# Optimization experiments

Measured on AMD Instinct MI355X. Metric: run time of the kernel, lower is better.

Reference implementation:

```python
import jax, jax.numpy as jnp
import numpy as np

B = 8192          # batch (tokens)
D_LAT = 1024      # latent_dim
D_EMB = 1024      # embed_dim
D = D_LAT + D_EMB # input_dim = 2048
E = 8             # num_experts
K = 2             # top-k


def setup_inputs() -> dict:
    key = jax.random.key(0)
    ks = jax.random.split(key, 6)
    s = 1.0 / np.sqrt(D)  # PyTorch nn.Linear init bound
    return {
        "x": jax.random.normal(ks[0], (B, D_LAT), dtype=jnp.float32),
        "y": jax.random.normal(ks[1], (B, D_EMB), dtype=jnp.float32),
        # expert Linear weights [E, out=D, in=D] and biases [E, D]
        "W_experts": jax.random.uniform(ks[2], (E, D, D), jnp.float32, -s, s),
        "b_experts": jax.random.uniform(ks[3], (E, D), jnp.float32, -s, s),
        # gate Linear weight [E, D] and bias [E]
        "W_gate": jax.random.uniform(ks[4], (E, D), jnp.float32, -s, s),
        "b_gate": jax.random.uniform(ks[5], (E,), jnp.float32, -s, s),
    }


def reference(x, y, W_experts, b_experts, W_gate, b_gate):
    # inp: [B, D]
    inp = jnp.concatenate([x, y], axis=1)
    # gating (eval mode: no noise): [B, E]
    gate_logits = inp @ W_gate.T + b_gate
    # top-k values/indices (sorted descending, matching torch.topk): [B, K]
    topk_val, topk_idx = jax.lax.top_k(gate_logits, K)
    topk_gates = jax.nn.softmax(topk_val, axis=1)  # [B, K]
    # dense all-expert outputs, matching original per-expert loop: [B, E, D]
    all_out = jnp.einsum('bd,eod->beo', inp, W_experts) + b_experts[None, :, :]
    # gather top-k expert outputs: [B, K, D]
    topk_out = jnp.take_along_axis(all_out, topk_idx[:, :, None], axis=1)
    # gate-weighted combine: [B, D]
    fused = jnp.sum(topk_out * topk_gates[:, :, None], axis=1)
    return fused
```

## Files before the change

kernel.cpp:

```cpp
#include <hip/hip_runtime.h>
#include <stdint.h>

typedef __attribute__((ext_vector_type(4))) float f32x4;
typedef __attribute__((ext_vector_type(8))) short short8v;
typedef __attribute__((ext_vector_type(8))) unsigned short ushort8v;
typedef __attribute__((ext_vector_type(4))) unsigned short ushort4v;

#define NB 8192
#define ND 2048
#define NE 8
#define NT 32

__device__ __forceinline__ unsigned short f2bf(float f) {
    union { float f; uint32_t u; } c; c.f = f;
    uint32_t u = c.u;
    u = u + 0x7FFFu + ((u >> 16) & 1u);
    return (unsigned short)(u >> 16);
}

__global__ __launch_bounds__(256) void cvt_w_kernel(const float* __restrict__ W,
                                                    unsigned short* __restrict__ Wb) {
    size_t i = ((size_t)blockIdx.x * 256 + threadIdx.x) * 8;
    float4 a = *(const float4*)(W + i);
    float4 b = *(const float4*)(W + i + 4);
    ushort8v o;
    o[0] = f2bf(a.x); o[1] = f2bf(a.y); o[2] = f2bf(a.z); o[3] = f2bf(a.w);
    o[4] = f2bf(b.x); o[5] = f2bf(b.y); o[6] = f2bf(b.z); o[7] = f2bf(b.w);
    *(ushort8v*)(Wb + i) = o;
}

__global__ __launch_bounds__(256) void gatecvt_kernel(const float* __restrict__ x,
                                                      const float* __restrict__ y,
                                                      const float* __restrict__ Wg,
                                                      const float* __restrict__ bg,
                                                      unsigned short* __restrict__ inpb,
                                                      int* __restrict__ tkidx,
                                                      float* __restrict__ tkg) {
    const int wave = threadIdx.x >> 6, lane = threadIdx.x & 63;
    const int b = blockIdx.x * 4 + wave;
    const float* xb = x + (size_t)b * 1024;
    const float* yb = y + (size_t)b * 1024;
    unsigned short* ob = inpb + (size_t)b * ND;
    double acc[NE] = {0, 0, 0, 0, 0, 0, 0, 0};
#pragma unroll
    for (int it = 0; it < 8; it++) {
        const int d = it * 256 + lane * 4;
        float4 v = (it < 4) ? *(const float4*)(xb + d) : *(const float4*)(yb + (d - 1024));
        ushort4v o;
        o[0] = f2bf(v.x); o[1] = f2bf(v.y); o[2] = f2bf(v.z); o[3] = f2bf(v.w);
        *(ushort4v*)(ob + d) = o;
#pragma unroll
        for (int e = 0; e < NE; e++) {
            float4 w = *(const float4*)(Wg + e * ND + d);
            acc[e] += (double)v.x * (double)w.x + (double)v.y * (double)w.y
                    + (double)v.z * (double)w.z + (double)v.w * (double)w.w;
        }
    }
#pragma unroll
    for (int e = 0; e < NE; e++) {
        double s = acc[e];
#pragma unroll
        for (int o = 32; o >= 1; o >>= 1) s += __shfl_xor(s, o, 64);
        acc[e] = s;
    }
    if (lane == 0) {
        double v0 = -1e300, v1 = -1e300; int i0 = 0, i1 = 1;
#pragma unroll
        for (int e = 0; e < NE; e++) {
            double val = acc[e] + (double)bg[e];
            if (val > v0)      { v1 = v0; i1 = i0; v0 = val; i0 = e; }
            else if (val > v1) { v1 = val; i1 = e; }
        }
        double e1 = exp(v1 - v0);
        double inv = 1.0 / (1.0 + e1);
        tkidx[b * 2]     = i0;
        tkidx[b * 2 + 1] = i1;
        tkg[b * 2]       = (float)inv;
        tkg[b * 2 + 1]   = (float)(e1 * inv);
    }
}

__global__ __launch_bounds__(256) void hist_kernel(const int* __restrict__ tkidx,
                                                   int* __restrict__ hist) {
    const int p = blockIdx.x * 256 + threadIdx.x;
    const int wave = threadIdx.x >> 6, lane = threadIdx.x & 63;
    const int e = tkidx[p];
    __shared__ int cnt[4][8];
#pragma unroll
    for (int e2 = 0; e2 < 8; e2++) {
        unsigned long long m = __ballot(e == e2);
        if (lane == e2) cnt[wave][e2] = __popcll(m);
    }
    __syncthreads();
    if (threadIdx.x < 8)
        hist[blockIdx.x * 8 + threadIdx.x] =
            cnt[0][threadIdx.x] + cnt[1][threadIdx.x] + cnt[2][threadIdx.x] + cnt[3][threadIdx.x];
}

__global__ void scan_kernel(const int* __restrict__ hist, int* __restrict__ chunkbase,
                            int* __restrict__ meta) {
    __shared__ int total[8], off[8];
    const int t = threadIdx.x;
    if (t < 8) {
        int run = 0;
        for (int c = 0; c < 64; c++) { chunkbase[c * 8 + t] = run; run += hist[c * 8 + t]; }
        total[t] = run; meta[t] = run;
    }
    __syncthreads();
    if (t == 0) { int o = 0; for (int e = 0; e < 8; e++) { off[e] = o; meta[8 + e] = o; o += total[e]; } }
    __syncthreads();
    for (int i = t; i < 512; i += 64) chunkbase[i] += off[i & 7];
}

__global__ __launch_bounds__(256) void fill_kernel(const int* __restrict__ tkidx,
                                                   const float* __restrict__ tkg,
                                                   const int* __restrict__ chunkbase,
                                                   int* __restrict__ tok,
                                                   float* __restrict__ gat) {
    const int p = blockIdx.x * 256 + threadIdx.x;
    const int wave = threadIdx.x >> 6, lane = threadIdx.x & 63;
    const int e = tkidx[p];
    const float g = tkg[p];
    __shared__ int cnt[4][8];
    unsigned long long mym = 0;
#pragma unroll
    for (int e2 = 0; e2 < 8; e2++) {
        unsigned long long m = __ballot(e == e2);
        if (e == e2) mym = m;
        if (lane == e2) cnt[wave][e2] = __popcll(m);
    }
    __syncthreads();
    int basep = chunkbase[blockIdx.x * 8 + e];
    for (int w = 0; w < wave; w++) basep += cnt[w][e];
    const int rank = __popcll(mym & ((1ull << lane) - 1ull));
    tok[basep + rank] = p;
    gat[basep + rank] = g;
}

__global__ __launch_bounds__(256) void combine_kernel(float* __restrict__ out,
                                                      const float* __restrict__ part1) {
    const size_t stride = (size_t)gridDim.x * 256 * 4;
    for (size_t i = ((size_t)blockIdx.x * 256 + threadIdx.x) * 4;
         i < (size_t)NB * ND; i += stride) {
        f32x4 a = *(const f32x4*)(out + i);
        f32x4 b = *(const f32x4*)(part1 + i);
        a = a + b;
        *(f32x4*)(out + i) = a;
    }
}

#define GLD16(gp, lp) __builtin_amdgcn_global_load_lds( \
    (const __attribute__((address_space(1))) uint32_t*)(gp), \
    (__attribute__((address_space(3))) uint32_t*)(lp), 16, 0, 0)

template <bool STORE>
__global__ __launch_bounds__(512, 2) void moe_gemm_kernel(
    const unsigned short* __restrict__ Ab,
    const unsigned short* __restrict__ Wb,
    const float* __restrict__ bias,
    const int* __restrict__ tok,
    const float* __restrict__ gat,
    const int* __restrict__ meta,
    float* __restrict__ out0,
    float* __restrict__ out1)
{
    const int e = blockIdx.z;
    const int cnt = meta[e];
    const int row0 = blockIdx.y * 256;
    if (row0 >= cnt) return;
    const int col0 = blockIdx.x * 256;
    const int base = meta[8 + e];

    __shared__ __align__(16) unsigned short S[2][4][128][64];

    const int tid  = threadIdx.x;
    const int wv   = tid >> 6;
    const int lane = tid & 63;
    const int wr = wv >> 2, wcn = wv & 3;
    const int fr = lane & 15, kh = lane >> 4;

    const int srow = tid >> 3;
    const int cg8  = ((tid & 7) ^ (srow & 7)) * 8;
    const unsigned short* wbase = Wb + (size_t)e * ND * ND;
    const unsigned short* aptr[2][2];
    const unsigned short* bptr[2][2];
#pragma unroll
    for (int h = 0; h < 2; h++)
#pragma unroll
        for (int i = 0; i < 2; i++) {
            int rt = h * 128 + i * 64 + srow;
            int gr = row0 + rt; if (gr > cnt - 1) gr = cnt - 1;
            aptr[h][i] = Ab + (size_t)(tok[base + gr] >> 1) * ND + cg8;
            bptr[h][i] = wbase + (size_t)(col0 + rt) * ND + cg8;
        }

#define STAGE_A(SB, SM, SK) do { \
    GLD16(aptr[SM][0] + (SK), (char*)&S[SB][SM][0][0] + tid * 16); \
    GLD16(aptr[SM][1] + (SK), (char*)&S[SB][SM][0][0] + tid * 16 + 8192); } while (0)
#define STAGE_B(SB, SN, SK) do { \
    GLD16(bptr[SN][0] + (SK), (char*)&S[SB][2 + SN][0][0] + tid * 16); \
    GLD16(bptr[SN][1] + (SK), (char*)&S[SB][2 + SN][0][0] + tid * 16 + 8192); } while (0)
#define STAGE_ALL(SB, SK) do { \
    STAGE_A(SB, 0, SK); STAGE_B(SB, 0, SK); STAGE_B(SB, 1, SK); STAGE_A(SB, 1, SK); } while (0)

    f32x4 acc[8][4];
#pragma unroll
    for (int m = 0; m < 8; m++)
#pragma unroll
        for (int n = 0; n < 4; n++) acc[m][n] = f32x4{0.f, 0.f, 0.f, 0.f};

    const int arow = wr * 64 + fr;
    int ca[2];
#pragma unroll
    for (int ks = 0; ks < 2; ks++) ca[ks] = ((ks * 4 + kh) ^ (fr & 7)) * 8;

#define LD_A(PB, PM, ML, KS) (*(const short8v*)&S[PB][PM][arow + (ML) * 16][ca[KS]])
#define LD_B(PB, N, KS)      (*(const short8v*)&S[PB][2 + ((N) >> 1)][wcn * 32 + ((N) & 1) * 16 + fr][ca[KS]])
#define MFMA16(MQ) do { \
    __builtin_amdgcn_s_setprio(1); \
    _Pragma("unroll") \
    for (int ml = 0; ml < 4; ml++) \
        _Pragma("unroll") \
        for (int n = 0; n < 4; n++) \
            acc[(MQ) * 4 + ml][n] = __builtin_amdgcn_mfma_f32_16x16x32_bf16( \
                ar[ml], br[n], acc[(MQ) * 4 + ml][n], 0, 0, 0); \
    __builtin_amdgcn_s_setprio(0); \
    __builtin_amdgcn_sched_barrier(0); \
} while (0)

#define BODY(PB) do { \
    short8v ar[4], br[4]; \
    _Pragma("unroll") \
    for (int i = 0; i < 4; i++) ar[i] = LD_A(PB, 0, i, 0); \
    _Pragma("unroll") \
    for (int i = 0; i < 4; i++) br[i] = LD_B(PB, i, 0); \
    MFMA16(0); \
    _Pragma("unroll") \
    for (int i = 0; i < 4; i++) ar[i] = LD_A(PB, 1, i, 0); \
    MFMA16(1); \
    _Pragma("unroll") \
    for (int i = 0; i < 4; i++) ar[i] = LD_A(PB, 0, i, 1); \
    _Pragma("unroll") \
    for (int i = 0; i < 4; i++) br[i] = LD_B(PB, i, 1); \
    MFMA16(0); \
    _Pragma("unroll") \
    for (int i = 0; i < 4; i++) ar[i] = LD_A(PB, 1, i, 1); \
    MFMA16(1); \
} while (0)

    STAGE_ALL(0, 0);
    __syncthreads();

    for (int t = 0; t < NT; t += 2) {
        if (t + 1 < NT) STAGE_ALL(1, (t + 1) * 64);
        BODY(0);
        __syncthreads();
        if (t + 2 < NT) STAGE_ALL(0, (t + 2) * 64);
        BODY(1);
        __syncthreads();
    }

    int   coln[4];
    float bv[4];
#pragma unroll
    for (int n = 0; n < 4; n++) {
        coln[n] = col0 + (n >> 1) * 128 + wcn * 32 + (n & 1) * 16 + fr;
        bv[n] = bias[e * ND + coln[n]];
    }
#pragma unroll
    for (int m = 0; m < 8; m++) {
        const int rbase = row0 + (m >> 2) * 128 + wr * 64 + (m & 3) * 16 + kh * 4;
#pragma unroll
        for (int j = 0; j < 4; j++) {
            const int R = rbase + j;
            if (R < cnt) {
                const int pr = tok[base + R];
                const float g = gat[base + R];
                float* orow = ((STORE && (pr & 1)) ? out1 : out0) + (size_t)(pr >> 1) * ND;
#pragma unroll
                for (int n = 0; n < 4; n++) {
                    const float v = g * (acc[m][n][j] + bv[n]);
                    if (STORE) orow[coln[n]] = v;
                    else       atomicAdd(&orow[coln[n]], v);
                }
            }
        }
    }
#undef BODY
#undef MFMA16
#undef LD_A
#undef LD_B
#undef STAGE_ALL
#undef STAGE_A
#undef STAGE_B
}

extern "C" void kernel_launch(void* const* d_in, const int* in_sizes, int n_in,
                              void* d_out, int out_size, void* d_ws, size_t ws_size,
                              hipStream_t stream) {
    const float* x  = (const float*)d_in[0];
    const float* y  = (const float*)d_in[1];
    const float* We = (const float*)d_in[2];
    const float* be = (const float*)d_in[3];
    const float* Wg = (const float*)d_in[4];
    const float* bg = (const float*)d_in[5];
    float* out = (float*)d_out;

    char* ws = (char*)d_ws;
    int*   meta  = (int*)ws;
    int*   hist  = (int*)(ws + 256);
    int*   cbase = (int*)(ws + 256 + 2048);
    int*   tkidx = (int*)(ws + 8192);
    float* tkg   = (float*)(ws + 8192 + 65536);
    int*   tok   = (int*)(ws + 8192 + 2 * 65536);
    float* gat   = (float*)(ws + 8192 + 3 * 65536);
    const size_t off_inpb = 8192 + 4 * 65536;
    const size_t off_wb   = off_inpb + (size_t)NB * ND * 2;
    const size_t off_p1   = off_wb + (size_t)NE * ND * ND * 2;
    const size_t needed   = off_p1 + (size_t)NB * ND * 4;
    unsigned short* inpb = (unsigned short*)(ws + off_inpb);
    unsigned short* wb   = (unsigned short*)(ws + off_wb);
    float*          part1 = (float*)(ws + off_p1);
    const bool store_mode = (ws_size >= needed);

    cvt_w_kernel<<<16384, 256, 0, stream>>>(We, wb);
    gatecvt_kernel<<<2048, 256, 0, stream>>>(x, y, Wg, bg, inpb, tkidx, tkg);
    hist_kernel<<<64, 256, 0, stream>>>(tkidx, hist);
    scan_kernel<<<1, 64, 0, stream>>>(hist, cbase, meta);
    fill_kernel<<<64, 256, 0, stream>>>(tkidx, tkg, cbase, tok, gat);
    if (store_mode) {
        moe_gemm_kernel<true><<<dim3(8, 32, 8), 512, 0, stream>>>(inpb, wb, be, tok, gat, meta, out, part1);
        combine_kernel<<<2048, 256, 0, stream>>>(out, part1);
    } else {
        (void)hipMemsetAsync(d_out, 0, (size_t)NB * ND * sizeof(float), stream);
        moe_gemm_kernel<false><<<dim3(8, 32, 8), 512, 0, stream>>>(inpb, wb, be, tok, gat, meta, out, out);
    }
}
```

Baseline: 291.7 us.

## Merge routing kernels into one block and preload B fragments in GEMM

Result: slower. 446.1 us (+53.0%).

```diff
diff --git a/kernel.cpp b/kernel.cpp
--- a/kernel.cpp
+++ b/kernel.cpp
@@ -80,61 +80,48 @@
     }
 }
 
-__global__ __launch_bounds__(256) void hist_kernel(const int* __restrict__ tkidx,
-                                                   int* __restrict__ hist) {
-    const int p = blockIdx.x * 256 + threadIdx.x;
-    const int wave = threadIdx.x >> 6, lane = threadIdx.x & 63;
-    const int e = tkidx[p];
-    __shared__ int cnt[4][8];
+__global__ __launch_bounds__(1024) void bucket_kernel(const int* __restrict__ tkidx,
+                                                      const float* __restrict__ tkg,
+                                                      int* __restrict__ meta,
+                                                      int* __restrict__ tok,
+                                                      float* __restrict__ gat) {
+    __shared__ int hist[1024][8];
+    __shared__ int ebase[8];
+    const int t = threadIdx.x;
+    int loc[16];
+#pragma unroll
+    for (int i = 0; i < 16; i++) loc[i] = tkidx[t * 16 + i];
 #pragma unroll
     for (int e2 = 0; e2 < 8; e2++) {
-        unsigned long long m = __ballot(e == e2);
-        if (lane == e2) cnt[wave][e2] = __popcll(m);
+        int c = 0;
+#pragma unroll
+        for (int i = 0; i < 16; i++) c += (loc[i] == e2) ? 1 : 0;
+        hist[t][e2] = c;
     }
     __syncthreads();
-    if (threadIdx.x < 8)
-        hist[blockIdx.x * 8 + threadIdx.x] =
-            cnt[0][threadIdx.x] + cnt[1][threadIdx.x] + cnt[2][threadIdx.x] + cnt[3][threadIdx.x];
-}
-
-__global__ void scan_kernel(const int* __restrict__ hist, int* __restrict__ chunkbase,
-                            int* __restrict__ meta) {
-    __shared__ int total[8], off[8];
-    const int t = threadIdx.x;
     if (t < 8) {
         int run = 0;
-        for (int c = 0; c < 64; c++) { chunkbase[c * 8 + t] = run; run += hist[c * 8 + t]; }
-        total[t] = run; meta[t] = run;
+        for (int j = 0; j < 1024; j++) { int v = hist[j][t]; hist[j][t] = run; run += v; }
+        meta[t] = run;
     }
     __syncthreads();
-    if (t == 0) { int o = 0; for (int e = 0; e < 8; e++) { off[e] = o; meta[8 + e] = o; o += total[e]; } }
+    if (t == 0) {
+        int o = 0;
+        for (int e = 0; e < 8; e++) { ebase[e] = o; meta[8 + e] = o; o += meta[e]; }
+    }
     __syncthreads();
-    for (int i = t; i < 512; i += 64) chunkbase[i] += off[i & 7];
-}
-
-__global__ __launch_bounds__(256) void fill_kernel(const int* __restrict__ tkidx,
-                                                   const float* __restrict__ tkg,
-                                                   const int* __restrict__ chunkbase,
-                                                   int* __restrict__ tok,
-                                                   float* __restrict__ gat) {
-    const int p = blockIdx.x * 256 + threadIdx.x;
-    const int wave = threadIdx.x >> 6, lane = threadIdx.x & 63;
-    const int e = tkidx[p];
-    const float g = tkg[p];
-    __shared__ int cnt[4][8];
-    unsigned long long mym = 0;
 #pragma unroll
     for (int e2 = 0; e2 < 8; e2++) {
-        unsigned long long m = __ballot(e == e2);
-        if (e == e2) mym = m;
-        if (lane == e2) cnt[wave][e2] = __popcll(m);
-    }
-    __syncthreads();
-    int basep = chunkbase[blockIdx.x * 8 + e];
-    for (int w = 0; w < wave; w++) basep += cnt[w][e];
-    const int rank = __popcll(mym & ((1ull << lane) - 1ull));
-    tok[basep + rank] = p;
-    gat[basep + rank] = g;
+        int pp = ebase[e2] + hist[t][e2];
+#pragma unroll
+        for (int i = 0; i < 16; i++) {
+            if (loc[i] == e2) {
+                tok[pp] = t * 16 + i;
+                gat[pp] = tkg[t * 16 + i];
+                pp++;
+            }
+        }
+    }
 }
 
 __global__ __launch_bounds__(256) void combine_kernel(float* __restrict__ out,
@@ -201,7 +188,7 @@
     GLD16(bptr[SN][0] + (SK), (char*)&S[SB][2 + SN][0][0] + tid * 16); \
     GLD16(bptr[SN][1] + (SK), (char*)&S[SB][2 + SN][0][0] + tid * 16 + 8192); } while (0)
 #define STAGE_ALL(SB, SK) do { \
-    STAGE_A(SB, 0, SK); STAGE_B(SB, 0, SK); STAGE_B(SB, 1, SK); STAGE_A(SB, 1, SK); } while (0)
+    STAGE_B(SB, 0, SK); STAGE_B(SB, 1, SK); STAGE_A(SB, 0, SK); STAGE_A(SB, 1, SK); } while (0)
 
     f32x4 acc[8][4];
 #pragma unroll
@@ -216,36 +203,36 @@
 
 #define LD_A(PB, PM, ML, KS) (*(const short8v*)&S[PB][PM][arow + (ML) * 16][ca[KS]])
 #define LD_B(PB, N, KS)      (*(const short8v*)&S[PB][2 + ((N) >> 1)][wcn * 32 + ((N) & 1) * 16 + fr][ca[KS]])
-#define MFMA16(MQ) do { \
+#define MFMA16(MQ, AR, BR) do { \
     __builtin_amdgcn_s_setprio(1); \
     _Pragma("unroll") \
     for (int ml = 0; ml < 4; ml++) \
         _Pragma("unroll") \
         for (int n = 0; n < 4; n++) \
             acc[(MQ) * 4 + ml][n] = __builtin_amdgcn_mfma_f32_16x16x32_bf16( \
-                ar[ml], br[n], acc[(MQ) * 4 + ml][n], 0, 0, 0); \
+                AR[ml], BR[n], acc[(MQ) * 4 + ml][n], 0, 0, 0); \
     __builtin_amdgcn_s_setprio(0); \
     __builtin_amdgcn_sched_barrier(0); \
 } while (0)
 
 #define BODY(PB) do { \
-    short8v ar[4], br[4]; \
+    short8v ar[4], brA[4], brB[4]; \
+    _Pragma("unroll") \
+    for (int n = 0; n < 4; n++) brA[n] = LD_B(PB, n, 0); \
+    _Pragma("unroll") \
+    for (int n = 0; n < 4; n++) brB[n] = LD_B(PB, n, 1); \
     _Pragma("unroll") \
     for (int i = 0; i < 4; i++) ar[i] = LD_A(PB, 0, i, 0); \
-    _Pragma("unroll") \
-    for (int i = 0; i < 4; i++) br[i] = LD_B(PB, i, 0); \
-    MFMA16(0); \
+    MFMA16(0, ar, brA); \
     _Pragma("unroll") \
     for (int i = 0; i < 4; i++) ar[i] = LD_A(PB, 1, i, 0); \
-    MFMA16(1); \
+    MFMA16(1, ar, brA); \
     _Pragma("unroll") \
     for (int i = 0; i < 4; i++) ar[i] = LD_A(PB, 0, i, 1); \
-    _Pragma("unroll") \
-    for (int i = 0; i < 4; i++) br[i] = LD_B(PB, i, 1); \
-    MFMA16(0); \
+    MFMA16(0, ar, brB); \
     _Pragma("unroll") \
     for (int i = 0; i < 4; i++) ar[i] = LD_A(PB, 1, i, 1); \
-    MFMA16(1); \
+    MFMA16(1, ar, brB); \
 } while (0)
 
     STAGE_ALL(0, 0);
@@ -308,8 +295,6 @@
 
     char* ws = (char*)d_ws;
     int*   meta  = (int*)ws;
-    int*   hist  = (int*)(ws + 256);
-    int*   cbase = (int*)(ws + 256 + 2048);
     int*   tkidx = (int*)(ws + 8192);
     float* tkg   = (float*)(ws + 8192 + 65536);
     int*   tok   = (int*)(ws + 8192 + 2 * 65536);
@@ -325,9 +310,7 @@
 
     cvt_w_kernel<<<16384, 256, 0, stream>>>(We, wb);
     gatecvt_kernel<<<2048, 256, 0, stream>>>(x, y, Wg, bg, inpb, tkidx, tkg);
-    hist_kernel<<<64, 256, 0, stream>>>(tkidx, hist);
-    scan_kernel<<<1, 64, 0, stream>>>(hist, cbase, meta);
-    fill_kernel<<<64, 256, 0, stream>>>(tkidx, tkg, cbase, tok, gat);
+    bucket_kernel<<<1, 1024, 0, stream>>>(tkidx, tkg, meta, tok, gat);
     if (store_mode) {
         moe_gemm_kernel<true><<<dim3(8, 32, 8), 512, 0, stream>>>(inpb, wb, be, tok, gat, meta, out, part1);
         combine_kernel<<<2048, 256, 0, stream>>>(out, part1);
```
